# Kernel optimization log

Hardware: AMD Instinct MI355X
Metric: run time of the kernel (lower is better)

The kernel has to match this reference:

```python
import jax, jax.numpy as jnp
import numpy as np

N = 100000   # nodes of ntype 'gene'
E = 800000   # edges per metapath
D = 256      # input_dim == output_dim
H = 4        # attn heads
C = D // H   # out_channels per head
M = 2        # num metapaths (tail relations = M + 1, last = self)


def _lrelu(x):
    return jnp.where(x >= 0, x, 0.2 * x)


def _segment_softmax(logits, seg, num_segments):
    # logits: [E, H], seg: [E] int targets
    mx = jax.ops.segment_max(logits, seg, num_segments=num_segments)
    mx = jnp.where(jnp.isfinite(mx), mx, 0.0)  # empty segments -> 0
    ex = jnp.exp(logits - mx[seg])
    den = jax.ops.segment_sum(ex, seg, num_segments=num_segments)
    return ex / (den[seg] + 1e-16)


def setup_inputs() -> dict:
    key = jax.random.key(0)
    ks = jax.random.split(key, 10)
    s = 1.0 / np.sqrt(D)
    return {
        "x": jax.random.normal(ks[0], (N, D), dtype=jnp.float32),
        "edge_index0": jax.random.randint(ks[1], (2, E), 0, N, dtype=jnp.int32),
        "edge_index1": jax.random.randint(ks[2], (2, E), 0, N, dtype=jnp.int32),
        "W_l": jax.random.normal(ks[3], (D, D), dtype=jnp.float32) * s,
        "b_l": jnp.zeros((D,), dtype=jnp.float32),
        "W_r": jax.random.normal(ks[4], (D, D), dtype=jnp.float32) * s,
        "b_r": jnp.zeros((D,), dtype=jnp.float32),
        "attn": jax.random.normal(ks[5], (M, H, 2 * C), dtype=jnp.float32) * (1.0 / np.sqrt(2 * C)),
        "rel_attn_l": jax.random.normal(ks[6], (H, C), dtype=jnp.float32) * (1.0 / np.sqrt(C)),
        "rel_attn_r": jax.random.normal(ks[7], (H, C), dtype=jnp.float32) * (1.0 / np.sqrt(C)),
    }


def reference(x, edge_index0, edge_index1, W_l, b_l, W_r, b_r, attn, rel_attn_l, rel_attn_r):
    # projections -> [N, H, C]  (eval mode: dropout/batchnorm off)
    l = (x @ W_l.T + b_l).reshape(N, H, C)
    r = (x @ W_r.T + b_r).reshape(N, H, C)

    # attn split: first C for x_i (target, r-proj), last C for x_j (source, l-proj);
    # leaky_relu is elementwise so the concat+dot separates exactly.
    def agg(edge_index, m_idx):
        src, tgt = edge_index[0], edge_index[1]
        a_i = jnp.einsum('ehc,hc->eh', _lrelu(r[tgt]), attn[m_idx, :, :C])
        a_j = jnp.einsum('ehc,hc->eh', _lrelu(l[src]), attn[m_idx, :, C:])
        alpha = _segment_softmax(a_i + a_j, tgt, N)          # [E, H]
        msg = l[src] * alpha[:, :, None]                      # [E, H, C]
        return jax.ops.segment_sum(msg, tgt, num_segments=N)  # [N, H, C]

    out0 = agg(edge_index0, 0)
    out1 = agg(edge_index1, 1)
    emb = jnp.stack([out0, out1, r], axis=1)                  # [N, M+1, H, C]

    # relation-level beta attention (get_beta_weights)
    alpha_l = jnp.einsum('nhc,hc->nh', r, rel_attn_l)         # [N, H]
    alpha_r = jnp.einsum('nrhc,hc->nrh', emb, rel_attn_r)     # [N, M+1, H]
    beta = jax.nn.softmax(_lrelu(alpha_l[:, None, :] + alpha_r), axis=1)

    h = (emb * beta[..., None]).sum(axis=1).reshape(N, D)
    return jax.nn.relu(h)
```

## Files before the change

### kernel.cpp

```cpp
#include <hip/hip_runtime.h>
#include <hip/hip_bf16.h>
#include <math.h>

#define D_ 256
#define H_ 4
#define C_ 64

typedef __attribute__((ext_vector_type(8))) short short8;
typedef __attribute__((ext_vector_type(4))) float f32x4;

__device__ inline float lrelu(float v) { return v >= 0.f ? v : 0.2f * v; }

__device__ inline unsigned short f2b(float f) {
    unsigned u = __float_as_uint(f);
    u = (u + 0x7FFFu + ((u >> 16) & 1u)) >> 16;
    return (unsigned short)u;
}
__device__ inline float b2f(unsigned short u) {
    return __uint_as_float(((unsigned)u) << 16);
}

#define GLDS(src, dst) __builtin_amdgcn_global_load_lds(                      \
    (const __attribute__((address_space(1))) void*)(src),                     \
    (__attribute__((address_space(3))) void*)(dst), 16, 0, 0)

__global__ __launch_bounds__(256) void convert_w(
    const float* __restrict__ Wl, const float* __restrict__ Wr,
    unsigned short* __restrict__ Wb)
{
    int i4 = blockIdx.x * 256 + threadIdx.x;
    float4 v = (i4 < 16384) ? ((const float4*)Wl)[i4]
                            : ((const float4*)Wr)[i4 - 16384];
    ushort4 u;
    u.x = f2b(v.x); u.y = f2b(v.y); u.z = f2b(v.z); u.w = f2b(v.w);
    ((ushort4*)Wb)[i4] = u;
}

__device__ __forceinline__ void stage_a(const float* __restrict__ x, float* dst,
                                        int bm, int k0, int wv, int lane, int Mrows)
{
#pragma unroll
    for (int p = 0; p < 4; p++) {
        int ci = (p * 4 + wv) * 64 + lane;
        int row = ci >> 3, cc = ci & 7;
        int gr = bm + row; if (gr >= Mrows) gr = Mrows - 1;
        const float* src = x + (size_t)gr * 256 + k0 + ((cc ^ (row & 7)) << 2);
        GLDS(src, (char*)dst + (size_t)(p * 4 + wv) * 1024);
    }
}
__device__ __forceinline__ void stage_b(const unsigned short* __restrict__ W,
                                        unsigned short* dst, int bn, int k0,
                                        int wv, int lane)
{
#pragma unroll
    for (int p = 0; p < 2; p++) {
        int ci = (p * 4 + wv) * 64 + lane;
        int col = ci >> 2, cc = ci & 3;
        const unsigned short* src = W + (size_t)(bn + col) * 256 + k0 +
                                    ((cc ^ ((col >> 1) & 3)) << 3);
        GLDS(src, (char*)dst + (size_t)(p * 4 + wv) * 1024);
    }
}

template <bool RB16>
__global__ __launch_bounds__(256) void gemm_hist(
    const float* __restrict__ x, const unsigned short* __restrict__ Wb,
    const float* __restrict__ b_l, const float* __restrict__ b_r,
    const float* __restrict__ attn, const float* __restrict__ rel_l,
    const float* __restrict__ rel_r,
    unsigned short* __restrict__ lout, void* __restrict__ rout,
    float2* __restrict__ ej2, float* __restrict__ al, float* __restrict__ rd,
    const int* __restrict__ ei0, const int* __restrict__ ei1,
    int* __restrict__ hist,
    int Mrows, int nblk, int E_)
{
    const int tid = threadIdx.x;

    if ((int)blockIdx.x >= nblk) {
        int e = ((int)blockIdx.x - nblk) * 256 + tid;
        if (e < E_) {
            atomicAdd(&hist[ei0[E_ + e]], 1);
            atomicAdd(&hist[Mrows + ei1[E_ + e]], 1);
        }
        return;
    }

    int hw = blockIdx.x;
    int orig = hw;
    if ((nblk & 7) == 0) {
        int cpx = nblk >> 3;
        orig = (hw & 7) * cpx + (hw >> 3);
    }
    const int sel = (orig & 3) >> 1;
    const int bn = (orig & 1) * 128;
    const int bm = (orig >> 2) * 128;

    __shared__ float As[2][128 * 32];
    __shared__ unsigned short Bs[2][128 * 32];
    const int lane = tid & 63, wv = tid >> 6;
    const int wr = wv >> 1, wc = wv & 1;
    const unsigned short* W = Wb + (size_t)sel * 65536;

    f32x4 acc[4][4];
#pragma unroll
    for (int m = 0; m < 4; m++)
#pragma unroll
        for (int n = 0; n < 4; n++) acc[m][n] = (f32x4)0.f;

    stage_a(x, As[0], bm, 0, wv, lane, Mrows);
    stage_b(W, Bs[0], bn, 0, wv, lane);
    __syncthreads();

    int cur = 0;
#pragma unroll
    for (int t = 0; t < 8; t++) {
        if (t < 7) {
            stage_a(x, As[cur ^ 1], bm, (t + 1) * 32, wv, lane, Mrows);
            stage_b(W, Bs[cur ^ 1], bn, (t + 1) * 32, wv, lane);
        }
        short8 bfr[4];
#pragma unroll
        for (int n = 0; n < 4; n++) {
            int col = wc * 64 + n * 16 + (lane & 15);
            int sc = (lane >> 4) ^ ((col >> 1) & 3);
            bfr[n] = *(const short8*)&Bs[cur][col * 32 + sc * 8];
        }
        short8 afr[4];
#pragma unroll
        for (int m = 0; m < 4; m++) {
            int row = wr * 64 + m * 16 + (lane & 15);
            int c0 = (lane >> 4) * 2;
            const float* ap = &As[cur][row * 32];
            float4 f0 = *(const float4*)&ap[(c0 ^ (row & 7)) << 2];
            float4 f1 = *(const float4*)&ap[((c0 + 1) ^ (row & 7)) << 2];
            union { short8 v; __hip_bfloat162 b2[4]; } u;
            u.b2[0] = __float22bfloat162_rn(make_float2(f0.x, f0.y));
            u.b2[1] = __float22bfloat162_rn(make_float2(f0.z, f0.w));
            u.b2[2] = __float22bfloat162_rn(make_float2(f1.x, f1.y));
            u.b2[3] = __float22bfloat162_rn(make_float2(f1.z, f1.w));
            afr[m] = u.v;
        }
#pragma unroll
        for (int m = 0; m < 4; m++)
#pragma unroll
            for (int n = 0; n < 4; n++)
                acc[m][n] = __builtin_amdgcn_mfma_f32_16x16x32_bf16(
                    afr[m], bfr[n], acc[m][n], 0, 0, 0);
        __syncthreads();
        cur ^= 1;
    }

    const float* bias = sel ? b_r : b_l;
    const int NH = Mrows * H_;
    const int h = (bn >> 6) + wc;
    float bv[4], w0[4], w1[4], w2[4];
    int gcol[4];
#pragma unroll
    for (int n = 0; n < 4; n++) {
        int c = n * 16 + (lane & 15);
        gcol[n] = bn + wc * 64 + c;
        bv[n] = bias[gcol[n]];
        if (sel == 0) {
            w0[n] = attn[(0 * H_ + h) * 128 + 64 + c];
            w1[n] = attn[(1 * H_ + h) * 128 + 64 + c];
            w2[n] = rel_r[h * C_ + c];
        } else {
            w0[n] = rel_l[h * C_ + c];
            w1[n] = rel_r[h * C_ + c];
        }
    }
#pragma unroll
    for (int m = 0; m < 4; m++) {
#pragma unroll
        for (int q = 0; q < 4; q++) {
            int grow = bm + wr * 64 + m * 16 + (lane >> 4) * 4 + q;
            bool ok = grow < Mrows;
            float p0 = 0.f, p1 = 0.f, p2 = 0.f;
#pragma unroll
            for (int n = 0; n < 4; n++) {
                float v = acc[m][n][q] + bv[n];
                if (ok) {
                    if (sel == 0) {
                        lout[(size_t)grow * 256 + gcol[n]] = f2b(v);
                    } else {
                        if (RB16) ((unsigned short*)rout)[(size_t)grow * 256 + gcol[n]] = f2b(v);
                        else      ((float*)rout)[(size_t)grow * 256 + gcol[n]] = v;
                    }
                }
                if (sel == 0) {
                    float lr = lrelu(v);
                    p0 = fmaf(lr, w0[n], p0);
                    p1 = fmaf(lr, w1[n], p1);
                    p2 = fmaf(v, w2[n], p2);
                } else {
                    p0 = fmaf(v, w0[n], p0);
                    p1 = fmaf(v, w1[n], p1);
                }
            }
#pragma unroll
            for (int off = 1; off < 16; off <<= 1) {
                p0 += __shfl_xor(p0, off);
                p1 += __shfl_xor(p1, off);
                if (sel == 0) p2 += __shfl_xor(p2, off);
            }
            if (ok && (lane & 15) == 0) {
                int nh = grow * H_ + h;
                if (sel == 0) {
                    float e0 = __expf(p0), e1 = __expf(p1);
                    ej2[nh]      = make_float2(e0, e0 * p2);
                    ej2[NH + nh] = make_float2(e1, e1 * p2);
                } else {
                    al[nh] = p0;
                    rd[nh] = p1;
                }
            }
        }
    }
}

__global__ __launch_bounds__(256) void scan_a(
    const int* __restrict__ hist, int* __restrict__ segoff,
    int* __restrict__ bsum, int Nn)
{
    int m = blockIdx.y;
    int gid = blockIdx.x * 256 + threadIdx.x;
    int lane = threadIdx.x & 63, wid = threadIdx.x >> 6;
    int v = (gid < Nn) ? hist[m * Nn + gid] : 0;
    int incl = v;
#pragma unroll
    for (int off = 1; off < 64; off <<= 1) {
        int u = __shfl_up(incl, off);
        if (lane >= off) incl += u;
    }
    __shared__ int ws[4], wo[4];
    if (lane == 63) ws[wid] = incl;
    __syncthreads();
    if (threadIdx.x == 0) {
        int run = 0;
#pragma unroll
        for (int i = 0; i < 4; i++) { wo[i] = run; run += ws[i]; }
        bsum[m * 512 + blockIdx.x] = run;
    }
    __syncthreads();
    if (gid < Nn) segoff[m * Nn + gid] = incl - v + wo[wid];
}

__global__ __launch_bounds__(512) void scan_b(int* __restrict__ bsum, int nb)
{
    int m = blockIdx.x;
    int* b = bsum + m * 512;
    int tid = threadIdx.x, lane = tid & 63, wid = tid >> 6;
    int v = (tid < nb) ? b[tid] : 0;
    int incl = v;
#pragma unroll
    for (int off = 1; off < 64; off <<= 1) {
        int u = __shfl_up(incl, off);
        if (lane >= off) incl += u;
    }
    __shared__ int ws[8], wo[8];
    if (lane == 63) ws[wid] = incl;
    __syncthreads();
    if (tid == 0) {
        int run = 0;
#pragma unroll
        for (int i = 0; i < 8; i++) { wo[i] = run; run += ws[i]; }
    }
    __syncthreads();
    if (tid < nb) b[tid] = incl - v + wo[wid];
}

__global__ __launch_bounds__(256) void edge_scatter(
    const int* __restrict__ ei0, const int* __restrict__ ei1,
    const int* __restrict__ segoff, const int* __restrict__ bsum,
    int* __restrict__ cursor, int* __restrict__ srcs, int E_, int Nn)
{
    int e = blockIdx.x * 256 + threadIdx.x;
    if (e >= E_) return;
    int t0 = ei0[E_ + e];
    int p0 = segoff[t0] + bsum[t0 >> 8] + atomicAdd(&cursor[t0], 1);
    srcs[p0] = ei0[e];
    int t1 = ei1[E_ + e];
    int p1 = segoff[Nn + t1] + bsum[512 + (t1 >> 8)] + atomicAdd(&cursor[Nn + t1], 1);
    srcs[E_ + p1] = ei1[e];
}

template <bool RB16>
__global__ __launch_bounds__(256) void aggregate(
    const int* __restrict__ hist, const int* __restrict__ segoff,
    const int* __restrict__ bsum,
    const int* __restrict__ srcs, const float2* __restrict__ ej2,
    const float* __restrict__ al, const float* __restrict__ rd,
    const void* __restrict__ rv, const unsigned short* __restrict__ l,
    float* __restrict__ out, int Nn, int E_)
{
    int lane = threadIdx.x & 63;
    int t = blockIdx.x * 4 + (threadIdx.x >> 6);
    if (t >= Nn) return;
    int h = lane >> 4;
    int NH = Nn * H_;
    int nh = t * H_ + h;

    float4 rrow;
    if (RB16) {
        ushort4 ru = ((const ushort4*)rv)[(size_t)t * 64 + lane];
        rrow = make_float4(b2f(ru.x), b2f(ru.y), b2f(ru.z), b2f(ru.w));
    } else {
        rrow = ((const float4*)rv)[(size_t)t * 64 + lane];
    }
    float a = al[nh];
    float rdv = rd[nh];

    float4 accm[2];
    float denm[2], pnm[2];
#pragma unroll
    for (int m = 0; m < 2; m++) {
        const int* sp = srcs + (size_t)m * E_;
        const float2* ep = ej2 + (size_t)m * NH;
        int beg = segoff[m * Nn + t] + bsum[m * 512 + (t >> 8)];
        int deg = hist[m * Nn + t];

        float4 aA = make_float4(0.f, 0.f, 0.f, 0.f);
        float4 aB = make_float4(0.f, 0.f, 0.f, 0.f);
        float dA = 0.f, dB = 0.f, pA = 0.f, pB = 0.f;
        int j = 0;
#pragma unroll 2
        for (; j + 1 < deg; j += 2) {
            int s0 = sp[beg + j];
            int s1 = sp[beg + j + 1];
            float2 v0 = ep[(size_t)s0 * H_ + h];
            float2 v1 = ep[(size_t)s1 * H_ + h];
            ushort4 l0 = *(const ushort4*)&l[(size_t)s0 * D_ + lane * 4];
            ushort4 l1 = *(const ushort4*)&l[(size_t)s1 * D_ + lane * 4];
            dA += v0.x; pA += v0.y;
            dB += v1.x; pB += v1.y;
            aA.x = fmaf(b2f(l0.x), v0.x, aA.x);
            aA.y = fmaf(b2f(l0.y), v0.x, aA.y);
            aA.z = fmaf(b2f(l0.z), v0.x, aA.z);
            aA.w = fmaf(b2f(l0.w), v0.x, aA.w);
            aB.x = fmaf(b2f(l1.x), v1.x, aB.x);
            aB.y = fmaf(b2f(l1.y), v1.x, aB.y);
            aB.z = fmaf(b2f(l1.z), v1.x, aB.z);
            aB.w = fmaf(b2f(l1.w), v1.x, aB.w);
        }
        if (j < deg) {
            int s0 = sp[beg + j];
            float2 v0 = ep[(size_t)s0 * H_ + h];
            ushort4 l0 = *(const ushort4*)&l[(size_t)s0 * D_ + lane * 4];
            dA += v0.x; pA += v0.y;
            aA.x = fmaf(b2f(l0.x), v0.x, aA.x);
            aA.y = fmaf(b2f(l0.y), v0.x, aA.y);
            aA.z = fmaf(b2f(l0.z), v0.x, aA.z);
            aA.w = fmaf(b2f(l0.w), v0.x, aA.w);
        }
        accm[m] = make_float4(aA.x + aB.x, aA.y + aB.y, aA.z + aB.z, aA.w + aB.w);
        denm[m] = dA + dB;
        pnm[m] = pA + pB;
    }

    float b0 = lrelu(a + pnm[0] / (denm[0] + 1e-16f));
    float b1 = lrelu(a + pnm[1] / (denm[1] + 1e-16f));
    float b2 = lrelu(a + rdv);
    float mm = fmaxf(b0, fmaxf(b1, b2));
    float e0 = __expf(b0 - mm), e1 = __expf(b1 - mm), e2 = __expf(b2 - mm);
    float inv = 1.f / (e0 + e1 + e2);
    float wm0 = e0 * inv / (denm[0] + 1e-16f);
    float wm1 = e1 * inv / (denm[1] + 1e-16f);
    float b2v = e2 * inv;

    float4 o;
    o.x = fmaxf(fmaf(wm0, accm[0].x, fmaf(wm1, accm[1].x, b2v * rrow.x)), 0.f);
    o.y = fmaxf(fmaf(wm0, accm[0].y, fmaf(wm1, accm[1].y, b2v * rrow.y)), 0.f);
    o.z = fmaxf(fmaf(wm0, accm[0].z, fmaf(wm1, accm[1].z, b2v * rrow.z)), 0.f);
    o.w = fmaxf(fmaf(wm0, accm[0].w, fmaf(wm1, accm[1].w, b2v * rrow.w)), 0.f);
    *(float4*)&out[(size_t)t * D_ + lane * 4] = o;
}

extern "C" void kernel_launch(void* const* d_in, const int* in_sizes, int n_in,
                              void* d_out, int out_size, void* d_ws, size_t ws_size,
                              hipStream_t stream) {
    const float* x     = (const float*)d_in[0];
    const int*   ei0   = (const int*)d_in[1];
    const int*   ei1   = (const int*)d_in[2];
    const float* W_l   = (const float*)d_in[3];
    const float* b_l   = (const float*)d_in[4];
    const float* W_r   = (const float*)d_in[5];
    const float* b_r   = (const float*)d_in[6];
    const float* attn  = (const float*)d_in[7];
    const float* rel_l = (const float*)d_in[8];
    const float* rel_r = (const float*)d_in[9];
    float* out = (float*)d_out;

    const int Nn = in_sizes[0] / D_;
    const int E_ = in_sizes[1] / 2;
    const size_t ND = (size_t)Nn * D_;
    const int NH = Nn * H_;

    char* base = (char*)d_ws;
    unsigned short* l = (unsigned short*)base;      size_t off = ND * 2;
    float2* ej2  = (float2*)(base + off); off += (size_t)2 * NH * 8;
    float* al    = (float*)(base + off);  off += (size_t)NH * 4;
    float* rd    = (float*)(base + off);  off += (size_t)NH * 4;
    int* hist    = (int*)(base + off);    off += (size_t)2 * Nn * 4;
    int* cursor  = (int*)(base + off);    off += (size_t)2 * Nn * 4;
    int* segoff  = (int*)(base + off);    off += (size_t)2 * Nn * 4;
    int* bsum    = (int*)(base + off);    off += (size_t)1024 * 4;
    int* srcs    = (int*)(base + off);    off += (size_t)2 * E_ * 4;
    unsigned short* Wb = (unsigned short*)(base + off); off += (size_t)2 * 65536 * 2;
    unsigned short* rb = (unsigned short*)(base + off);
    const bool rb16 = (ws_size >= off + ND * 2);
    void* r_any = rb16 ? (void*)rb : (void*)out;

    hipMemsetAsync(hist, 0, (size_t)4 * Nn * 4, stream);

    convert_w<<<128, 256, 0, stream>>>(W_l, W_r, Wb);

    int rowTiles = (Nn + 127) / 128;
    int nblk = 4 * rowTiles;
    int eb = (E_ + 255) / 256;
    if (rb16)
        gemm_hist<true ><<<nblk + eb, 256, 0, stream>>>(
            x, Wb, b_l, b_r, attn, rel_l, rel_r, l, r_any, ej2, al, rd,
            ei0, ei1, hist, Nn, nblk, E_);
    else
        gemm_hist<false><<<nblk + eb, 256, 0, stream>>>(
            x, Wb, b_l, b_r, attn, rel_l, rel_r, l, r_any, ej2, al, rd,
            ei0, ei1, hist, Nn, nblk, E_);

    int nb = (Nn + 255) / 256;
    scan_a<<<dim3(nb, 2), 256, 0, stream>>>(hist, segoff, bsum, Nn);
    scan_b<<<2, 512, 0, stream>>>(bsum, nb);
    edge_scatter<<<eb, 256, 0, stream>>>(ei0, ei1, segoff, bsum, cursor, srcs, E_, Nn);

    if (rb16)
        aggregate<true ><<<(Nn + 3) / 4, 256, 0, stream>>>(
            hist, segoff, bsum, srcs, ej2, al, rd, r_any, l, out, Nn, E_);
    else
        aggregate<false><<<(Nn + 3) / 4, 256, 0, stream>>>(
            hist, segoff, bsum, srcs, ej2, al, rd, r_any, l, out, Nn, E_);
}
```

Before: 420.5 us.

## Pre-convert x to bf16 in a fused prep kernel and stage bf16 A tiles

Adds a fused prep kernel that converts the weights and x to bf16 and also computes the edge histogram, which was previously tacked onto the GEMM launch. The GEMM now stages bf16 A tiles directly into LDS, halving A-tile LDS traffic and removing per-iteration float-to-bf16 conversion. The r projection is now always kept in fp32 in the output buffer instead of a bf16 workspace copy. The cost is an extra full pass over x (read fp32, write bf16) before the GEMM, and the fp32 r buffer doubles the bytes the aggregate kernel reads for r.

```diff
diff --git a/kernel.cpp b/kernel.cpp
--- a/kernel.cpp
+++ b/kernel.cpp
@@ -24,20 +24,69 @@
     (const __attribute__((address_space(1))) void*)(src),                     \
     (__attribute__((address_space(3))) void*)(dst), 16, 0, 0)
 
-__global__ __launch_bounds__(256) void convert_w(
+__global__ __launch_bounds__(256) void convert_wx_hist(
     const float* __restrict__ Wl, const float* __restrict__ Wr,
-    unsigned short* __restrict__ Wb)
-{
-    int i4 = blockIdx.x * 256 + threadIdx.x;
-    float4 v = (i4 < 16384) ? ((const float4*)Wl)[i4]
-                            : ((const float4*)Wr)[i4 - 16384];
-    ushort4 u;
-    u.x = f2b(v.x); u.y = f2b(v.y); u.z = f2b(v.z); u.w = f2b(v.w);
-    ((ushort4*)Wb)[i4] = u;
-}
-
-__device__ __forceinline__ void stage_a(const float* __restrict__ x, float* dst,
-                                        int bm, int k0, int wv, int lane, int Mrows)
+    const float* __restrict__ x,
+    unsigned short* __restrict__ Wb, unsigned short* __restrict__ xb,
+    const int* __restrict__ ei0, const int* __restrict__ ei1,
+    int* __restrict__ hist, int Nn, int E_, int xblocks)
+{
+    int bid = blockIdx.x, tid = threadIdx.x;
+    if (bid < 128) {
+        int i4 = bid * 256 + tid;
+        float4 v = (i4 < 16384) ? ((const float4*)Wl)[i4]
+                                : ((const float4*)Wr)[i4 - 16384];
+        ushort4 u;
+        u.x = f2b(v.x); u.y = f2b(v.y); u.z = f2b(v.z); u.w = f2b(v.w);
+        ((ushort4*)Wb)[i4] = u;
+        return;
+    }
+    if (bid < 128 + xblocks) {
+        int i = (bid - 128) * 256 + tid;
+        if (i < Nn * 64) {
+            float4 v = ((const float4*)x)[i];
+            ushort4 u;
+            u.x = f2b(v.x); u.y = f2b(v.y); u.z = f2b(v.z); u.w = f2b(v.w);
+            ((ushort4*)xb)[i] = u;
+        }
+        return;
+    }
+    int e = (bid - 128 - xblocks) * 256 + tid;
+    if (e < E_) {
+        atomicAdd(&hist[ei0[E_ + e]], 1);
+        atomicAdd(&hist[Nn + ei1[E_ + e]], 1);
+    }
+}
+
+__device__ __forceinline__ void stage_a16(const unsigned short* __restrict__ xb,
+                                          unsigned short* dst, int bm, int k0,
+                                          int wv, int lane, int Mrows)
+{
+#pragma unroll
+    for (int p = 0; p < 2; p++) {
+        int ci = (p * 4 + wv) * 64 + lane;
+        int row = ci >> 2, cc = ci & 3;
+        int gr = bm + row; if (gr >= Mrows) gr = Mrows - 1;
+        const unsigned short* src = xb + (size_t)gr * 256 + k0 +
+                                    ((cc ^ ((row >> 1) & 3)) << 3);
+        GLDS(src, (char*)dst + (size_t)(p * 4 + wv) * 1024);
+    }
+}
+__device__ __forceinline__ void stage_b(const unsigned short* __restrict__ W,
+                                        unsigned short* dst, int bn, int k0,
+                                        int wv, int lane)
+{
+#pragma unroll
+    for (int p = 0; p < 2; p++) {
+        int ci = (p * 4 + wv) * 64 + lane;
+        int col = ci >> 2, cc = ci & 3;
+        const unsigned short* src = W + (size_t)(bn + col) * 256 + k0 +
+                                    ((cc ^ ((col >> 1) & 3)) << 3);
+        GLDS(src, (char*)dst + (size_t)(p * 4 + wv) * 1024);
+    }
+}
+__device__ __forceinline__ void stage_a32(const float* __restrict__ x, float* dst,
+                                          int bm, int k0, int wv, int lane, int Mrows)
 {
 #pragma unroll
     for (int p = 0; p < 4; p++) {
@@ -48,108 +97,16 @@
         GLDS(src, (char*)dst + (size_t)(p * 4 + wv) * 1024);
     }
 }
-__device__ __forceinline__ void stage_b(const unsigned short* __restrict__ W,
-                                        unsigned short* dst, int bn, int k0,
-                                        int wv, int lane)
-{
-#pragma unroll
-    for (int p = 0; p < 2; p++) {
-        int ci = (p * 4 + wv) * 64 + lane;
-        int col = ci >> 2, cc = ci & 3;
-        const unsigned short* src = W + (size_t)(bn + col) * 256 + k0 +
-                                    ((cc ^ ((col >> 1) & 3)) << 3);
-        GLDS(src, (char*)dst + (size_t)(p * 4 + wv) * 1024);
-    }
-}
-
-template <bool RB16>
-__global__ __launch_bounds__(256) void gemm_hist(
-    const float* __restrict__ x, const unsigned short* __restrict__ Wb,
+
+__device__ __forceinline__ void gemm_epilogue(
+    f32x4 (&acc)[4][4], int sel, int bm, int bn, int wr, int wc, int lane,
     const float* __restrict__ b_l, const float* __restrict__ b_r,
     const float* __restrict__ attn, const float* __restrict__ rel_l,
     const float* __restrict__ rel_r,
-    unsigned short* __restrict__ lout, void* __restrict__ rout,
+    unsigned short* __restrict__ lout, float* __restrict__ rout,
     float2* __restrict__ ej2, float* __restrict__ al, float* __restrict__ rd,
-    const int* __restrict__ ei0, const int* __restrict__ ei1,
-    int* __restrict__ hist,
-    int Mrows, int nblk, int E_)
-{
-    const int tid = threadIdx.x;
-
-    if ((int)blockIdx.x >= nblk) {
-        int e = ((int)blockIdx.x - nblk) * 256 + tid;
-        if (e < E_) {
-            atomicAdd(&hist[ei0[E_ + e]], 1);
-            atomicAdd(&hist[Mrows + ei1[E_ + e]], 1);
-        }
-        return;
-    }
-
-    int hw = blockIdx.x;
-    int orig = hw;
-    if ((nblk & 7) == 0) {
-        int cpx = nblk >> 3;
-        orig = (hw & 7) * cpx + (hw >> 3);
-    }
-    const int sel = (orig & 3) >> 1;
-    const int bn = (orig & 1) * 128;
-    const int bm = (orig >> 2) * 128;
-
-    __shared__ float As[2][128 * 32];
-    __shared__ unsigned short Bs[2][128 * 32];
-    const int lane = tid & 63, wv = tid >> 6;
-    const int wr = wv >> 1, wc = wv & 1;
-    const unsigned short* W = Wb + (size_t)sel * 65536;
-
-    f32x4 acc[4][4];
-#pragma unroll
-    for (int m = 0; m < 4; m++)
-#pragma unroll
-        for (int n = 0; n < 4; n++) acc[m][n] = (f32x4)0.f;
-
-    stage_a(x, As[0], bm, 0, wv, lane, Mrows);
-    stage_b(W, Bs[0], bn, 0, wv, lane);
-    __syncthreads();
-
-    int cur = 0;
-#pragma unroll
-    for (int t = 0; t < 8; t++) {
-        if (t < 7) {
-            stage_a(x, As[cur ^ 1], bm, (t + 1) * 32, wv, lane, Mrows);
-            stage_b(W, Bs[cur ^ 1], bn, (t + 1) * 32, wv, lane);
-        }
-        short8 bfr[4];
-#pragma unroll
-        for (int n = 0; n < 4; n++) {
-            int col = wc * 64 + n * 16 + (lane & 15);
-            int sc = (lane >> 4) ^ ((col >> 1) & 3);
-            bfr[n] = *(const short8*)&Bs[cur][col * 32 + sc * 8];
-        }
-        short8 afr[4];
-#pragma unroll
-        for (int m = 0; m < 4; m++) {
-            int row = wr * 64 + m * 16 + (lane & 15);
-            int c0 = (lane >> 4) * 2;
-            const float* ap = &As[cur][row * 32];
-            float4 f0 = *(const float4*)&ap[(c0 ^ (row & 7)) << 2];
-            float4 f1 = *(const float4*)&ap[((c0 + 1) ^ (row & 7)) << 2];
-            union { short8 v; __hip_bfloat162 b2[4]; } u;
-            u.b2[0] = __float22bfloat162_rn(make_float2(f0.x, f0.y));
-            u.b2[1] = __float22bfloat162_rn(make_float2(f0.z, f0.w));
-            u.b2[2] = __float22bfloat162_rn(make_float2(f1.x, f1.y));
-            u.b2[3] = __float22bfloat162_rn(make_float2(f1.z, f1.w));
-            afr[m] = u.v;
-        }
-#pragma unroll
-        for (int m = 0; m < 4; m++)
-#pragma unroll
-            for (int n = 0; n < 4; n++)
-                acc[m][n] = __builtin_amdgcn_mfma_f32_16x16x32_bf16(
-                    afr[m], bfr[n], acc[m][n], 0, 0, 0);
-        __syncthreads();
-        cur ^= 1;
-    }
-
+    int Mrows)
+{
     const float* bias = sel ? b_r : b_l;
     const int NH = Mrows * H_;
     const int h = (bn >> 6) + wc;
@@ -180,12 +137,8 @@
             for (int n = 0; n < 4; n++) {
                 float v = acc[m][n][q] + bv[n];
                 if (ok) {
-                    if (sel == 0) {
-                        lout[(size_t)grow * 256 + gcol[n]] = f2b(v);
-                    } else {
-                        if (RB16) ((unsigned short*)rout)[(size_t)grow * 256 + gcol[n]] = f2b(v);
-                        else      ((float*)rout)[(size_t)grow * 256 + gcol[n]] = v;
-                    }
+                    if (sel == 0) lout[(size_t)grow * 256 + gcol[n]] = f2b(v);
+                    else          rout[(size_t)grow * 256 + gcol[n]] = v;
                 }
                 if (sel == 0) {
                     float lr = lrelu(v);
@@ -218,6 +171,153 @@
     }
 }
 
+__global__ __launch_bounds__(256) void gemm_b16(
+    const unsigned short* __restrict__ xb, const unsigned short* __restrict__ Wb,
+    const float* __restrict__ b_l, const float* __restrict__ b_r,
+    const float* __restrict__ attn, const float* __restrict__ rel_l,
+    const float* __restrict__ rel_r,
+    unsigned short* __restrict__ lout, float* __restrict__ rout,
+    float2* __restrict__ ej2, float* __restrict__ al, float* __restrict__ rd,
+    int Mrows, int nblk)
+{
+    int hw = blockIdx.x;
+    int orig = hw;
+    if ((nblk & 7) == 0) {
+        int cpx = nblk >> 3;
+        orig = (hw & 7) * cpx + (hw >> 3);
+    }
+    const int sel = (orig & 3) >> 1;
+    const int bn = (orig & 1) * 128;
+    const int bm = (orig >> 2) * 128;
+
+    __shared__ unsigned short As[2][128 * 32];
+    __shared__ unsigned short Bs[2][128 * 32];
+    const int tid = threadIdx.x;
+    const int lane = tid & 63, wv = tid >> 6;
+    const int wr = wv >> 1, wc = wv & 1;
+    const unsigned short* W = Wb + (size_t)sel * 65536;
+
+    f32x4 acc[4][4];
+#pragma unroll
+    for (int m = 0; m < 4; m++)
+#pragma unroll
+        for (int n = 0; n < 4; n++) acc[m][n] = (f32x4)0.f;
+
+    stage_a16(xb, As[0], bm, 0, wv, lane, Mrows);
+    stage_b(W, Bs[0], bn, 0, wv, lane);
+    __syncthreads();
+
+    int cur = 0;
+#pragma unroll
+    for (int t = 0; t < 8; t++) {
+        if (t < 7) {
+            stage_a16(xb, As[cur ^ 1], bm, (t + 1) * 32, wv, lane, Mrows);
+            stage_b(W, Bs[cur ^ 1], bn, (t + 1) * 32, wv, lane);
+        }
+        short8 bfr[4], afr[4];
+#pragma unroll
+        for (int n = 0; n < 4; n++) {
+            int col = wc * 64 + n * 16 + (lane & 15);
+            int sc = (lane >> 4) ^ ((col >> 1) & 3);
+            bfr[n] = *(const short8*)&Bs[cur][col * 32 + sc * 8];
+        }
+#pragma unroll
+        for (int m = 0; m < 4; m++) {
+            int row = wr * 64 + m * 16 + (lane & 15);
+            int sa = (lane >> 4) ^ ((row >> 1) & 3);
+            afr[m] = *(const short8*)&As[cur][row * 32 + sa * 8];
+        }
+#pragma unroll
+        for (int m = 0; m < 4; m++)
+#pragma unroll
+            for (int n = 0; n < 4; n++)
+                acc[m][n] = __builtin_amdgcn_mfma_f32_16x16x32_bf16(
+                    afr[m], bfr[n], acc[m][n], 0, 0, 0);
+        __syncthreads();
+        cur ^= 1;
+    }
+    gemm_epilogue(acc, sel, bm, bn, wr, wc, lane, b_l, b_r, attn, rel_l, rel_r,
+                  lout, rout, ej2, al, rd, Mrows);
+}
+
+__global__ __launch_bounds__(256) void gemm_f32(
+    const float* __restrict__ x, const unsigned short* __restrict__ Wb,
+    const float* __restrict__ b_l, const float* __restrict__ b_r,
+    const float* __restrict__ attn, const float* __restrict__ rel_l,
+    const float* __restrict__ rel_r,
+    unsigned short* __restrict__ lout, float* __restrict__ rout,
+    float2* __restrict__ ej2, float* __restrict__ al, float* __restrict__ rd,
+    int Mrows, int nblk)
+{
+    int hw = blockIdx.x;
+    int orig = hw;
+    if ((nblk & 7) == 0) {
+        int cpx = nblk >> 3;
+        orig = (hw & 7) * cpx + (hw >> 3);
+    }
+    const int sel = (orig & 3) >> 1;
+    const int bn = (orig & 1) * 128;
+    const int bm = (orig >> 2) * 128;
+
+    __shared__ float As[2][128 * 32];
+    __shared__ unsigned short Bs[2][128 * 32];
+    const int tid = threadIdx.x;
+    const int lane = tid & 63, wv = tid >> 6;
+    const int wr = wv >> 1, wc = wv & 1;
+    const unsigned short* W = Wb + (size_t)sel * 65536;
+
+    f32x4 acc[4][4];
+#pragma unroll
+    for (int m = 0; m < 4; m++)
+#pragma unroll
+        for (int n = 0; n < 4; n++) acc[m][n] = (f32x4)0.f;
+
+    stage_a32(x, As[0], bm, 0, wv, lane, Mrows);
+    stage_b(W, Bs[0], bn, 0, wv, lane);
+    __syncthreads();
+
+    int cur = 0;
+#pragma unroll
+    for (int t = 0; t < 8; t++) {
+        if (t < 7) {
+            stage_a32(x, As[cur ^ 1], bm, (t + 1) * 32, wv, lane, Mrows);
+            stage_b(W, Bs[cur ^ 1], bn, (t + 1) * 32, wv, lane);
+        }
+        short8 bfr[4];
+#pragma unroll
+        for (int n = 0; n < 4; n++) {
+            int col = wc * 64 + n * 16 + (lane & 15);
+            int sc = (lane >> 4) ^ ((col >> 1) & 3);
+            bfr[n] = *(const short8*)&Bs[cur][col * 32 + sc * 8];
+        }
+        short8 afr[4];
+#pragma unroll
+        for (int m = 0; m < 4; m++) {
+            int row = wr * 64 + m * 16 + (lane & 15);
+            int c0 = (lane >> 4) * 2;
+            const float* ap = &As[cur][row * 32];
+            float4 f0 = *(const float4*)&ap[(c0 ^ (row & 7)) << 2];
+            float4 f1 = *(const float4*)&ap[((c0 + 1) ^ (row & 7)) << 2];
+            union { short8 v; __hip_bfloat162 b2[4]; } u;
+            u.b2[0] = __float22bfloat162_rn(make_float2(f0.x, f0.y));
+            u.b2[1] = __float22bfloat162_rn(make_float2(f0.z, f0.w));
+            u.b2[2] = __float22bfloat162_rn(make_float2(f1.x, f1.y));
+            u.b2[3] = __float22bfloat162_rn(make_float2(f1.z, f1.w));
+            afr[m] = u.v;
+        }
+#pragma unroll
+        for (int m = 0; m < 4; m++)
+#pragma unroll
+            for (int n = 0; n < 4; n++)
+                acc[m][n] = __builtin_amdgcn_mfma_f32_16x16x32_bf16(
+                    afr[m], bfr[n], acc[m][n], 0, 0, 0);
+        __syncthreads();
+        cur ^= 1;
+    }
+    gemm_epilogue(acc, sel, bm, bn, wr, wc, lane, b_l, b_r, attn, rel_l, rel_r,
+                  lout, rout, ej2, al, rd, Mrows);
+}
+
 __global__ __launch_bounds__(256) void scan_a(
     const int* __restrict__ hist, int* __restrict__ segoff,
     int* __restrict__ bsum, int Nn)
@@ -284,13 +384,12 @@
     srcs[E_ + p1] = ei1[e];
 }
 
-template <bool RB16>
 __global__ __launch_bounds__(256) void aggregate(
     const int* __restrict__ hist, const int* __restrict__ segoff,
     const int* __restrict__ bsum,
     const int* __restrict__ srcs, const float2* __restrict__ ej2,
     const float* __restrict__ al, const float* __restrict__ rd,
-    const void* __restrict__ rv, const unsigned short* __restrict__ l,
+    const float* __restrict__ rv, const unsigned short* __restrict__ l,
     float* __restrict__ out, int Nn, int E_)
 {
     int lane = threadIdx.x & 63;
@@ -300,13 +399,7 @@
     int NH = Nn * H_;
     int nh = t * H_ + h;
 
-    float4 rrow;
-    if (RB16) {
-        ushort4 ru = ((const ushort4*)rv)[(size_t)t * 64 + lane];
-        rrow = make_float4(b2f(ru.x), b2f(ru.y), b2f(ru.z), b2f(ru.w));
-    } else {
-        rrow = ((const float4*)rv)[(size_t)t * 64 + lane];
-    }
+    float4 rrow = *(const float4*)&rv[(size_t)t * D_ + lane * 4];
     float a = al[nh];
     float rdv = rd[nh];
 
@@ -406,35 +499,30 @@
     int* bsum    = (int*)(base + off);    off += (size_t)1024 * 4;
     int* srcs    = (int*)(base + off);    off += (size_t)2 * E_ * 4;
     unsigned short* Wb = (unsigned short*)(base + off); off += (size_t)2 * 65536 * 2;
-    unsigned short* rb = (unsigned short*)(base + off);
-    const bool rb16 = (ws_size >= off + ND * 2);
-    void* r_any = rb16 ? (void*)rb : (void*)out;
+    unsigned short* xb = (unsigned short*)(base + off);
+    const bool xb16 = (ws_size >= off + ND * 2);
 
     hipMemsetAsync(hist, 0, (size_t)4 * Nn * 4, stream);
 
-    convert_w<<<128, 256, 0, stream>>>(W_l, W_r, Wb);
+    int eb = (E_ + 255) / 256;
+    int xblocks = xb16 ? (Nn * 64 + 255) / 256 : 0;
+    convert_wx_hist<<<128 + xblocks + eb, 256, 0, stream>>>(
+        W_l, W_r, x, Wb, xb, ei0, ei1, hist, Nn, E_, xblocks);
 
     int rowTiles = (Nn + 127) / 128;
     int nblk = 4 * rowTiles;
-    int eb = (E_ + 255) / 256;
-    if (rb16)
-        gemm_hist<true ><<<nblk + eb, 256, 0, stream>>>(
-            x, Wb, b_l, b_r, attn, rel_l, rel_r, l, r_any, ej2, al, rd,
-            ei0, ei1, hist, Nn, nblk, E_);
+    if (xb16)
+        gemm_b16<<<nblk, 256, 0, stream>>>(
+            xb, Wb, b_l, b_r, attn, rel_l, rel_r, l, out, ej2, al, rd, Nn, nblk);
     else
-        gemm_hist<false><<<nblk + eb, 256, 0, stream>>>(
-            x, Wb, b_l, b_r, attn, rel_l, rel_r, l, r_any, ej2, al, rd,
-            ei0, ei1, hist, Nn, nblk, E_);
+        gemm_f32<<<nblk, 256, 0, stream>>>(
+            x, Wb, b_l, b_r, attn, rel_l, rel_r, l, out, ej2, al, rd, Nn, nblk);
 
     int nb = (Nn + 255) / 256;
     scan_a<<<dim3(nb, 2), 256, 0, stream>>>(hist, segoff, bsum, Nn);
     scan_b<<<2, 512, 0, stream>>>(bsum, nb);
     edge_scatter<<<eb, 256, 0, stream>>>(ei0, ei1, segoff, bsum, cursor, srcs, E_, Nn);
 
-    if (rb16)
-        aggregate<true ><<<(Nn + 3) / 4, 256, 0, stream>>>(
-            hist, segoff, bsum, srcs, ej2, al, rd, r_any, l, out, Nn, E_);
-    else
-        aggregate<false><<<(Nn + 3) / 4, 256, 0, stream>>>(
-            hist, segoff, bsum, srcs, ej2, al, rd, r_any, l, out, Nn, E_);
-}
+    aggregate<<<(Nn + 3) / 4, 256, 0, stream>>>(
+        hist, segoff, bsum, srcs, ej2, al, rd, out, l, out, Nn, E_);
+}
```

Result: slower. 446.2 us (+6.1%).

## Compute both L and R projections per block to reuse staged x tile

Applied to the files above, without the earlier changes.

Each GEMM block now computes both the W_l and W_r projections for its row and column tile, staging both weight tiles in LDS and keeping two accumulator sets. This halves the number of GEMM blocks and the number of times each fp32 x tile is loaded and converted to bf16. Padding the block count to a multiple of 8 makes the XCD-swizzle remap unconditional. The cost is double the accumulator registers and more LDS per block, with launch bounds asking for 2 blocks per SM, which may limit occupancy or cause spills.

```diff
diff --git a/kernel.cpp b/kernel.cpp
--- a/kernel.cpp
+++ b/kernel.cpp
@@ -48,22 +48,24 @@
         GLDS(src, (char*)dst + (size_t)(p * 4 + wv) * 1024);
     }
 }
-__device__ __forceinline__ void stage_b(const unsigned short* __restrict__ W,
-                                        unsigned short* dst, int bn, int k0,
-                                        int wv, int lane)
-{
-#pragma unroll
-    for (int p = 0; p < 2; p++) {
+__device__ __forceinline__ void stage_b2(const unsigned short* __restrict__ Wb,
+                                         unsigned short* dst, int bn, int k0,
+                                         int wv, int lane)
+{
+#pragma unroll
+    for (int p = 0; p < 4; p++) {
         int ci = (p * 4 + wv) * 64 + lane;
-        int col = ci >> 2, cc = ci & 3;
-        const unsigned short* src = W + (size_t)(bn + col) * 256 + k0 +
+        int selb = ci >> 9, cj = ci & 511;
+        int col = cj >> 2, cc = cj & 3;
+        const unsigned short* src = Wb + (size_t)selb * 65536 +
+                                    (size_t)(bn + col) * 256 + k0 +
                                     ((cc ^ ((col >> 1) & 3)) << 3);
         GLDS(src, (char*)dst + (size_t)(p * 4 + wv) * 1024);
     }
 }
 
 template <bool RB16>
-__global__ __launch_bounds__(256) void gemm_hist(
+__global__ __launch_bounds__(256, 2) void gemm_hist(
     const float* __restrict__ x, const unsigned short* __restrict__ Wb,
     const float* __restrict__ b_l, const float* __restrict__ b_r,
     const float* __restrict__ attn, const float* __restrict__ rel_l,
@@ -72,12 +74,12 @@
     float2* __restrict__ ej2, float* __restrict__ al, float* __restrict__ rd,
     const int* __restrict__ ei0, const int* __restrict__ ei1,
     int* __restrict__ hist,
-    int Mrows, int nblk, int E_)
+    int Mrows, int nblkPad, int E_)
 {
     const int tid = threadIdx.x;
 
-    if ((int)blockIdx.x >= nblk) {
-        int e = ((int)blockIdx.x - nblk) * 256 + tid;
+    if ((int)blockIdx.x >= nblkPad) {
+        int e = ((int)blockIdx.x - nblkPad) * 256 + tid;
         if (e < E_) {
             atomicAdd(&hist[ei0[E_ + e]], 1);
             atomicAdd(&hist[Mrows + ei1[E_ + e]], 1);
@@ -86,29 +88,26 @@
     }
 
     int hw = blockIdx.x;
-    int orig = hw;
-    if ((nblk & 7) == 0) {
-        int cpx = nblk >> 3;
-        orig = (hw & 7) * cpx + (hw >> 3);
-    }
-    const int sel = (orig & 3) >> 1;
+    int cpx = nblkPad >> 3;
+    int orig = (hw & 7) * cpx + (hw >> 3);
+    int rt = orig >> 1;
+    if (rt * 128 >= Mrows) return;
     const int bn = (orig & 1) * 128;
-    const int bm = (orig >> 2) * 128;
+    const int bm = rt * 128;
 
     __shared__ float As[2][128 * 32];
-    __shared__ unsigned short Bs[2][128 * 32];
+    __shared__ unsigned short Bs[2][2][128 * 32];
     const int lane = tid & 63, wv = tid >> 6;
     const int wr = wv >> 1, wc = wv & 1;
-    const unsigned short* W = Wb + (size_t)sel * 65536;
-
-    f32x4 acc[4][4];
+
+    f32x4 accL[4][4], accR[4][4];
 #pragma unroll
     for (int m = 0; m < 4; m++)
 #pragma unroll
-        for (int n = 0; n < 4; n++) acc[m][n] = (f32x4)0.f;
+        for (int n = 0; n < 4; n++) { accL[m][n] = (f32x4)0.f; accR[m][n] = (f32x4)0.f; }
 
     stage_a(x, As[0], bm, 0, wv, lane, Mrows);
-    stage_b(W, Bs[0], bn, 0, wv, lane);
+    stage_b2(Wb, &Bs[0][0][0], bn, 0, wv, lane);
     __syncthreads();
 
     int cur = 0;
@@ -116,16 +115,16 @@
     for (int t = 0; t < 8; t++) {
         if (t < 7) {
             stage_a(x, As[cur ^ 1], bm, (t + 1) * 32, wv, lane, Mrows);
-            stage_b(W, Bs[cur ^ 1], bn, (t + 1) * 32, wv, lane);
-        }
-        short8 bfr[4];
+            stage_b2(Wb, &Bs[cur ^ 1][0][0], bn, (t + 1) * 32, wv, lane);
+        }
+        short8 bfrL[4], bfrR[4], afr[4];
 #pragma unroll
         for (int n = 0; n < 4; n++) {
             int col = wc * 64 + n * 16 + (lane & 15);
             int sc = (lane >> 4) ^ ((col >> 1) & 3);
-            bfr[n] = *(const short8*)&Bs[cur][col * 32 + sc * 8];
-        }
-        short8 afr[4];
+            bfrL[n] = *(const short8*)&Bs[cur][0][col * 32 + sc * 8];
+            bfrR[n] = *(const short8*)&Bs[cur][1][col * 32 + sc * 8];
+        }
 #pragma unroll
         for (int m = 0; m < 4; m++) {
             int row = wr * 64 + m * 16 + (lane & 15);
@@ -143,31 +142,30 @@
 #pragma unroll
         for (int m = 0; m < 4; m++)
 #pragma unroll
-            for (int n = 0; n < 4; n++)
-                acc[m][n] = __builtin_amdgcn_mfma_f32_16x16x32_bf16(
-                    afr[m], bfr[n], acc[m][n], 0, 0, 0);
+            for (int n = 0; n < 4; n++) {
+                accL[m][n] = __builtin_amdgcn_mfma_f32_16x16x32_bf16(
+                    afr[m], bfrL[n], accL[m][n], 0, 0, 0);
+                accR[m][n] = __builtin_amdgcn_mfma_f32_16x16x32_bf16(
+                    afr[m], bfrR[n], accR[m][n], 0, 0, 0);
+            }
         __syncthreads();
         cur ^= 1;
     }
 
-    const float* bias = sel ? b_r : b_l;
     const int NH = Mrows * H_;
     const int h = (bn >> 6) + wc;
-    float bv[4], w0[4], w1[4], w2[4];
+    float bvl[4], bvr[4], w0[4], w1[4], w2[4], u0[4];
     int gcol[4];
 #pragma unroll
     for (int n = 0; n < 4; n++) {
         int c = n * 16 + (lane & 15);
         gcol[n] = bn + wc * 64 + c;
-        bv[n] = bias[gcol[n]];
-        if (sel == 0) {
-            w0[n] = attn[(0 * H_ + h) * 128 + 64 + c];
-            w1[n] = attn[(1 * H_ + h) * 128 + 64 + c];
-            w2[n] = rel_r[h * C_ + c];
-        } else {
-            w0[n] = rel_l[h * C_ + c];
-            w1[n] = rel_r[h * C_ + c];
-        }
+        bvl[n] = b_l[gcol[n]];
+        bvr[n] = b_r[gcol[n]];
+        w0[n] = attn[(0 * H_ + h) * 128 + 64 + c];
+        w1[n] = attn[(1 * H_ + h) * 128 + 64 + c];
+        w2[n] = rel_r[h * C_ + c];
+        u0[n] = rel_l[h * C_ + c];
     }
 #pragma unroll
     for (int m = 0; m < 4; m++) {
@@ -175,44 +173,38 @@
         for (int q = 0; q < 4; q++) {
             int grow = bm + wr * 64 + m * 16 + (lane >> 4) * 4 + q;
             bool ok = grow < Mrows;
-            float p0 = 0.f, p1 = 0.f, p2 = 0.f;
+            float p0 = 0.f, p1 = 0.f, p2 = 0.f, q0 = 0.f, q1 = 0.f;
 #pragma unroll
             for (int n = 0; n < 4; n++) {
-                float v = acc[m][n][q] + bv[n];
+                float vl = accL[m][n][q] + bvl[n];
+                float vr = accR[m][n][q] + bvr[n];
                 if (ok) {
-                    if (sel == 0) {
-                        lout[(size_t)grow * 256 + gcol[n]] = f2b(v);
-                    } else {
-                        if (RB16) ((unsigned short*)rout)[(size_t)grow * 256 + gcol[n]] = f2b(v);
-                        else      ((float*)rout)[(size_t)grow * 256 + gcol[n]] = v;
-                    }
+                    lout[(size_t)grow * 256 + gcol[n]] = f2b(vl);
+                    if (RB16) ((unsigned short*)rout)[(size_t)grow * 256 + gcol[n]] = f2b(vr);
+                    else      ((float*)rout)[(size_t)grow * 256 + gcol[n]] = vr;
                 }
-                if (sel == 0) {
-                    float lr = lrelu(v);
-                    p0 = fmaf(lr, w0[n], p0);
-                    p1 = fmaf(lr, w1[n], p1);
-                    p2 = fmaf(v, w2[n], p2);
-                } else {
-                    p0 = fmaf(v, w0[n], p0);
-                    p1 = fmaf(v, w1[n], p1);
-                }
+                float lr = lrelu(vl);
+                p0 = fmaf(lr, w0[n], p0);
+                p1 = fmaf(lr, w1[n], p1);
+                p2 = fmaf(vl, w2[n], p2);
+                q0 = fmaf(vr, u0[n], q0);
+                q1 = fmaf(vr, w2[n], q1);
             }
 #pragma unroll
             for (int off = 1; off < 16; off <<= 1) {
                 p0 += __shfl_xor(p0, off);
                 p1 += __shfl_xor(p1, off);
-                if (sel == 0) p2 += __shfl_xor(p2, off);
+                p2 += __shfl_xor(p2, off);
+                q0 += __shfl_xor(q0, off);
+                q1 += __shfl_xor(q1, off);
             }
             if (ok && (lane & 15) == 0) {
                 int nh = grow * H_ + h;
-                if (sel == 0) {
-                    float e0 = __expf(p0), e1 = __expf(p1);
-                    ej2[nh]      = make_float2(e0, e0 * p2);
-                    ej2[NH + nh] = make_float2(e1, e1 * p2);
-                } else {
-                    al[nh] = p0;
-                    rd[nh] = p1;
-                }
+                float e0 = __expf(p0), e1 = __expf(p1);
+                ej2[nh]      = make_float2(e0, e0 * p2);
+                ej2[NH + nh] = make_float2(e1, e1 * p2);
+                al[nh] = q0;
+                rd[nh] = q1;
             }
         }
     }
@@ -415,16 +407,17 @@
     convert_w<<<128, 256, 0, stream>>>(W_l, W_r, Wb);
 
     int rowTiles = (Nn + 127) / 128;
-    int nblk = 4 * rowTiles;
+    int nblk = 2 * rowTiles;
+    int nblkPad = (nblk + 7) & ~7;
     int eb = (E_ + 255) / 256;
     if (rb16)
-        gemm_hist<true ><<<nblk + eb, 256, 0, stream>>>(
+        gemm_hist<true ><<<nblkPad + eb, 256, 0, stream>>>(
             x, Wb, b_l, b_r, attn, rel_l, rel_r, l, r_any, ej2, al, rd,
-            ei0, ei1, hist, Nn, nblk, E_);
+            ei0, ei1, hist, Nn, nblkPad, E_);
     else
-        gemm_hist<false><<<nblk + eb, 256, 0, stream>>>(
+        gemm_hist<false><<<nblkPad + eb, 256, 0, stream>>>(
             x, Wb, b_l, b_r, attn, rel_l, rel_r, l, r_any, ej2, al, rd,
-            ei0, ei1, hist, Nn, nblk, E_);
+            ei0, ei1, hist, Nn, nblkPad, E_);
 
     int nb = (Nn + 255) / 256;
     scan_a<<<dim3(nb, 2), 256, 0, stream>>>(hist, segoff, bsum, Nn);
```

Result: faster. 395.7 us (median of 2 runs) (-5.9%).
